# Optimization experiments

Measured on AMD Instinct MI355X. Metric: run time of the kernel, lower is better.

## Reference

```python
import jax, jax.numpy as jnp
import numpy as np

F = 64  # dim_features
DIM_TASK = 32


def setup_inputs() -> dict:
    key = jax.random.key(0)
    ks = jax.random.split(key, 16)
    n_state, n_task, n_actor = 65536, 32768, 32768
    E_st, E_ta = 2_000_000, 1_000_000
    inp = {
        'x_state': jax.random.normal(ks[0], (n_state, F), jnp.float32),
        'x_task': jax.random.normal(ks[1], (n_task, F), jnp.float32),
        'x_actor': jax.random.normal(ks[2], (n_actor, F), jnp.float32),
        'edge_attr': jax.random.normal(ks[3], (E_st, 2), jnp.float32),
        # GINEConv edge linear: Linear(2 -> F)
        'We': jax.random.normal(ks[4], (2, F), jnp.float32) * 0.5,
        'be': jnp.zeros((F,), jnp.float32),
        # GinStandardMLP: Linear(F,F) -> ReLU -> Linear(F,F)
        'W1a': jax.random.normal(ks[5], (F, F), jnp.float32) / np.sqrt(F),
        'b1a': jnp.zeros((F,), jnp.float32),
        'W1b': jax.random.normal(ks[6], (F, F), jnp.float32) / np.sqrt(F),
        'b1b': jnp.zeros((F,), jnp.float32),
        # UnactivatedMLP: Linear(F,F) -> ReLU -> Linear(F,1)
        'W2a': jax.random.normal(ks[7], (F, F), jnp.float32) / np.sqrt(F),
        'b2a': jnp.zeros((F,), jnp.float32),
        'W2b': jax.random.normal(ks[8], (F, 1), jnp.float32) / np.sqrt(F),
        'b2b': jnp.zeros((1,), jnp.float32),
        'src_st': jax.random.randint(ks[9], (E_st,), 0, n_state, jnp.int32),
        'dst_st': jax.random.randint(ks[10], (E_st,), 0, n_task, jnp.int32),
        'src_ta': jax.random.randint(ks[11], (E_ta,), 0, n_task, jnp.int32),
        'dst_ta': jax.random.randint(ks[12], (E_ta,), 0, n_actor, jnp.int32),
    }
    return inp


def reference(x_state, x_task, x_actor, edge_attr, We, be, W1a, b1a, W1b, b1b,
              W2a, b2a, W2b, b2b, src_st, dst_st, src_ta, dst_ta):
    n_task = x_task.shape[0]
    n_actor = x_actor.shape[0]
    # --- GINEConv (eps=0): agg_i = sum_e relu(x_src[e] + lin(edge_attr[e])) ---
    msg = jax.nn.relu(x_state[src_st] + edge_attr @ We + be)  # [E_st, F]
    agg = jax.ops.segment_sum(msg, dst_st, num_segments=n_task)  # [n_task, F]
    h = x_task + agg  # (1+eps)*x_r + agg, eps=0
    # GinStandardMLP: Linear-ReLU-Linear
    x1 = jax.nn.relu(h @ W1a + b1a) @ W1b + b1b  # [n_task, F]
    # --- GINConv (eps=0): agg2_i = sum_e x1[src[e]] ---
    agg2 = jax.ops.segment_sum(x1[src_ta], dst_ta, num_segments=n_actor)  # [n_actor, F]
    h2 = x_actor + agg2
    # UnactivatedMLP: Linear-ReLU-Linear -> 1
    logits = jax.nn.relu(h2 @ W2a + b2a) @ W2b + b2b  # [n_actor, 1]
    return logits.reshape(-1, DIM_TASK)
```

## Files before the change

### kernel.cpp

```cpp
#include <hip/hip_runtime.h>

#define F 64
#define TILE 8192
#define NB 1024
#define ROWSB 32
#define CAP1 2560
#define CAP2 1408
#define HS 68

#define WP1AH 0
#define WP1AL 4096
#define WP1BH 8192
#define WP1BL 12288
#define WP2AH 16384
#define WP2AL 20480

typedef __attribute__((ext_vector_type(8))) short bf8;
typedef __attribute__((ext_vector_type(4))) float f4;
typedef __attribute__((ext_vector_type(2))) float fl2;

__device__ __forceinline__ unsigned short f2bf(float f) {
    unsigned u = __float_as_uint(f);
    unsigned r = u + 0x7fffu + ((u >> 16) & 1u);
    return (unsigned short)(r >> 16);
}
__device__ __forceinline__ float bf2f(unsigned short h) {
    return __uint_as_float((unsigned)h << 16);
}
__device__ __forceinline__ fl2 unpack2(unsigned d) {
    fl2 r;
    r.x = __uint_as_float(d << 16);
    r.y = __uint_as_float(d & 0xffff0000u);
    return r;
}

__device__ __forceinline__ int block_scan_1024(int c, int tid, int* scratch) {
    int lane = tid & 63, wv = tid >> 6;
    int s = c;
    #pragma unroll
    for (int off = 1; off < 64; off <<= 1) {
        int u = __shfl_up(s, off);
        if (lane >= off) s += u;
    }
    if (lane == 63) scratch[wv] = s;
    __syncthreads();
    if (tid < 64) {
        int ws = (tid < 16) ? scratch[tid] : 0;
        int t = ws;
        #pragma unroll
        for (int off = 1; off < 16; off <<= 1) {
            int u = __shfl_up(t, off);
            if (tid >= off) t += u;
        }
        if (tid < 16) scratch[16 + tid] = t - ws;
    }
    __syncthreads();
    return s - c + scratch[16 + wv];
}

__global__ __launch_bounds__(1024) void prep_kernel(
    const float4* __restrict__ xs4, ushort4* __restrict__ xsb4, int n4,
    const int* __restrict__ src1, const int* __restrict__ dst1,
    const float* __restrict__ ea, int E1,
    int* __restrict__ cur1, uint2* __restrict__ keyA1,
    const int* __restrict__ src2, const int* __restrict__ dst2, int E2,
    int* __restrict__ cur2, unsigned* __restrict__ keyA2,
    const float* __restrict__ W1a, const float* __restrict__ W1b,
    const float* __restrict__ W2a, ushort* __restrict__ wp,
    int nBin1, int nBin2)
{
    __shared__ uint2 stage[TILE];
    __shared__ int hist[NB], lcur[NB], comb[NB];
    __shared__ int scratch[32];
    int bid = blockIdx.x;
    int tid = threadIdx.x;

    if (bid == 0) {
        int fid = tid & 511;
        int col = fid & 15, quad = (fid >> 4) & 3, c = (fid >> 6) & 3, kh = (fid >> 8) & 1;
        const float* Wsrc = (tid < 512) ? W1a : W1b;
        ushort* dh = wp + ((tid < 512) ? WP1AH : WP1BH);
        ushort* dl = wp + ((tid < 512) ? WP1AL : WP1BL);
        #pragma unroll
        for (int j = 0; j < 8; ++j) {
            int k = kh * 32 + quad * 8 + j;
            float w = Wsrc[k * F + c * 16 + col];
            unsigned short hi = f2bf(w);
            dh[fid * 8 + j] = hi;
            dl[fid * 8 + j] = f2bf(w - bf2f(hi));
        }
        if (tid < 512) {
            #pragma unroll
            for (int j = 0; j < 8; ++j) {
                int k = kh * 32 + quad * 8 + j;
                float w = W2a[k * F + c * 16 + col];
                unsigned short hi = f2bf(w);
                wp[WP2AH + fid * 8 + j] = hi;
                wp[WP2AL + fid * 8 + j] = f2bf(w - bf2f(hi));
            }
        }
        return;
    }

    if (bid <= nBin1) {
        int base = (bid - 1) * TILE;
        int cnt = min(TILE, E1 - base);
        hist[tid] = 0;
        __syncthreads();
        int myb[8]; unsigned msd[8], mpk[8];
        #pragma unroll
        for (int j = 0; j < 8; ++j) {
            int idx = tid + 1024 * j;
            if (idx < cnt) {
                int d = dst1[base + idx];
                int s = src1[base + idx];
                float2 e2 = ((const float2* __restrict__)ea)[base + idx];
                myb[j] = d >> 5;
                msd[j] = ((unsigned)s << 16) | (unsigned)d;
                mpk[j] = ((unsigned)f2bf(e2.y) << 16) | (unsigned)f2bf(e2.x);
                atomicAdd(&hist[myb[j]], 1);
            } else myb[j] = -1;
        }
        __syncthreads();
        int c = hist[tid];
        int gb = CAP1 * tid + atomicAdd(&cur1[tid], c);
        int excl = block_scan_1024(c, tid, scratch);
        comb[tid] = gb - excl;
        lcur[tid] = excl;
        __syncthreads();
        #pragma unroll
        for (int j = 0; j < 8; ++j) {
            if (myb[j] >= 0) {
                int p = atomicAdd(&lcur[myb[j]], 1);
                stage[p] = make_uint2(msd[j], mpk[j]);
            }
        }
        __syncthreads();
        #pragma unroll
        for (int j = 0; j < 8; ++j) {
            int p = tid + 1024 * j;
            if (p < cnt) {
                uint2 f = stage[p];
                int b = (int)(f.x & 0xffffu) >> 5;
                keyA1[comb[b] + p] = f;
            }
        }
        return;
    }

    if (bid <= nBin1 + nBin2) {
        unsigned* ustage = (unsigned*)stage;
        int base = (bid - 1 - nBin1) * TILE;
        int cnt = min(TILE, E2 - base);
        hist[tid] = 0;
        __syncthreads();
        int myb[8]; unsigned msd[8];
        #pragma unroll
        for (int j = 0; j < 8; ++j) {
            int idx = tid + 1024 * j;
            if (idx < cnt) {
                int d = dst2[base + idx];
                int s = src2[base + idx];
                myb[j] = d >> 5;
                msd[j] = ((unsigned)s << 16) | (unsigned)d;
                atomicAdd(&hist[myb[j]], 1);
            } else myb[j] = -1;
        }
        __syncthreads();
        int c = hist[tid];
        int gb = CAP2 * tid + atomicAdd(&cur2[tid], c);
        int excl = block_scan_1024(c, tid, scratch);
        comb[tid] = gb - excl;
        lcur[tid] = excl;
        __syncthreads();
        #pragma unroll
        for (int j = 0; j < 8; ++j) {
            if (myb[j] >= 0) {
                int p = atomicAdd(&lcur[myb[j]], 1);
                ustage[p] = msd[j];
            }
        }
        __syncthreads();
        #pragma unroll
        for (int j = 0; j < 8; ++j) {
            int p = tid + 1024 * j;
            if (p < cnt) {
                unsigned f = ustage[p];
                int b = (int)(f & 0xffffu) >> 5;
                keyA2[comb[b] + p] = f;
            }
        }
        return;
    }

    {
        int i = (bid - 1 - nBin1 - nBin2) * 1024 + tid;
        if (i < n4) {
            float4 v = xs4[i];
            ushort4 o;
            o.x = f2bf(v.x); o.y = f2bf(v.y); o.z = f2bf(v.z); o.w = f2bf(v.w);
            xsb4[i] = o;
        }
    }
}

__global__ __launch_bounds__(512) void sg1_kernel(
    const uint2* __restrict__ keyA,
    const ushort* __restrict__ xsb,
    const float* __restrict__ x_task,
    const float* __restrict__ We, const float* __restrict__ be,
    const int* __restrict__ gcursor,
    const ushort* __restrict__ wp,
    const float* __restrict__ b1a, const float* __restrict__ b1b,
    ushort* __restrict__ x1b, int n)
{
    __shared__ uint2 lpay[CAP1];
    __shared__ int hh[ROWSB], rst[ROWSB], cur[ROWSB];
    __shared__ float htile[ROWSB * HS];
    __shared__ float ltile[2 * 16 * HS];
    int tid = threadIdx.x;
    int b = blockIdx.x;
    int cnt = min(gcursor[b], CAP1);
    const uint2* ka = keyA + (size_t)b * CAP1;

    uint2 myk[5];
    #pragma unroll
    for (int j = 0; j < 5; ++j) {
        int idx = tid + 512 * j;
        if (idx < cnt) myk[j] = ka[idx];
    }
    if (tid < ROWSB) hh[tid] = 0;
    __syncthreads();
    #pragma unroll
    for (int j = 0; j < 5; ++j) {
        int idx = tid + 512 * j;
        if (idx < cnt) atomicAdd(&hh[myk[j].x & 31u], 1);
    }
    __syncthreads();
    if (tid < 64) {
        int cc = (tid < ROWSB) ? hh[tid] : 0;
        int s = cc;
        #pragma unroll
        for (int off = 1; off < ROWSB; off <<= 1) {
            int u = __shfl_up(s, off);
            if (tid >= off) s += u;
        }
        if (tid < ROWSB) { rst[tid] = s - cc; cur[tid] = s - cc; }
    }
    __syncthreads();
    #pragma unroll
    for (int j = 0; j < 5; ++j) {
        int idx = tid + 512 * j;
        if (idx < cnt) {
            int p = atomicAdd(&cur[myk[j].x & 31u], 1);
            lpay[p] = myk[j];
        }
    }
    __syncthreads();

    int wave = tid >> 6, lane = tid & 63;
    int q = lane & 7, g = lane >> 3;
    int gid = (wave << 3) | g;
    int r   = gid >> 1;
    int h   = gid & 1;
    int row = b * ROWSB + r;

    fl2 w0p[4], w1p[4], bbp[4];
    {
        float4 a0 = ((const float4* __restrict__)We)[q * 2];
        float4 a1 = ((const float4* __restrict__)We)[q * 2 + 1];
        float4 c0 = ((const float4* __restrict__)(We + F))[q * 2];
        float4 c1 = ((const float4* __restrict__)(We + F))[q * 2 + 1];
        float4 d0 = ((const float4* __restrict__)be)[q * 2];
        float4 d1 = ((const float4* __restrict__)be)[q * 2 + 1];
        w0p[0] = (fl2){a0.x, a0.y}; w0p[1] = (fl2){a0.z, a0.w};
        w0p[2] = (fl2){a1.x, a1.y}; w0p[3] = (fl2){a1.z, a1.w};
        w1p[0] = (fl2){c0.x, c0.y}; w1p[1] = (fl2){c0.z, c0.w};
        w1p[2] = (fl2){c1.x, c1.y}; w1p[3] = (fl2){c1.z, c1.w};
        bbp[0] = (fl2){d0.x, d0.y}; bbp[1] = (fl2){d0.z, d0.w};
        bbp[2] = (fl2){d1.x, d1.y}; bbp[3] = (fl2){d1.z, d1.w};
    }
    const fl2 zero2 = {0.f, 0.f};

    int c  = hh[r];
    int m0 = (c + 1) >> 1;
    int sh = rst[r] + (h ? m0 : 0);
    int m  = h ? (c - m0) : m0;

    fl2 acc2[4];
    #pragma unroll
    for (int p = 0; p < 4; ++p) acc2[p] = zero2;

    unsigned pk0 = 0, pk1 = 0, pk2 = 0, pk3 = 0;
    uint4 xw0 = {0,0,0,0}, xw1 = {0,0,0,0}, xw2 = {0,0,0,0}, xw3 = {0,0,0,0};

    #define SG1_LOAD(J, K)                                                          \
    if ((K) < m) {                                                                  \
        uint2 t = lpay[sh + (K)];                                                   \
        pk##J = t.y;                                                                \
        xw##J = ((const uint4* __restrict__)(xsb + ((size_t)(t.x >> 16) << 6)))[q]; \
    }

    #define SG1_COMP(PK, XW)                                                        \
    {                                                                               \
        fl2 ex = {__uint_as_float((PK) << 16), __uint_as_float((PK) << 16)};        \
        fl2 ey = {__uint_as_float((PK) & 0xffff0000u),                              \
                  __uint_as_float((PK) & 0xffff0000u)};                             \
        fl2 cc, t2;                                                                 \
        cc = __builtin_elementwise_fma(ey, w1p[0], bbp[0]);                         \
        cc = __builtin_elementwise_fma(ex, w0p[0], cc);                             \
        t2 = unpack2((XW).x) + cc;                                                  \
        acc2[0] += __builtin_elementwise_max(t2, zero2);                            \
        cc = __builtin_elementwise_fma(ey, w1p[1], bbp[1]);                         \
        cc = __builtin_elementwise_fma(ex, w0p[1], cc);                             \
        t2 = unpack2((XW).y) + cc;                                                  \
        acc2[1] += __builtin_elementwise_max(t2, zero2);                            \
        cc = __builtin_elementwise_fma(ey, w1p[2], bbp[2]);                         \
        cc = __builtin_elementwise_fma(ex, w0p[2], cc);                             \
        t2 = unpack2((XW).z) + cc;                                                  \
        acc2[2] += __builtin_elementwise_max(t2, zero2);                            \
        cc = __builtin_elementwise_fma(ey, w1p[3], bbp[3]);                         \
        cc = __builtin_elementwise_fma(ex, w0p[3], cc);                             \
        t2 = unpack2((XW).w) + cc;                                                  \
        acc2[3] += __builtin_elementwise_max(t2, zero2);                            \
    }

    SG1_LOAD(0, 0)
    SG1_LOAD(1, 1)
    SG1_LOAD(2, 2)
    SG1_LOAD(3, 3)
    int i = 0;
    for (; i + 4 <= m; i += 4) {
        SG1_COMP(pk0, xw0) SG1_LOAD(0, i + 4)
        SG1_COMP(pk1, xw1) SG1_LOAD(1, i + 5)
        SG1_COMP(pk2, xw2) SG1_LOAD(2, i + 6)
        SG1_COMP(pk3, xw3) SG1_LOAD(3, i + 7)
    }
    if (i < m)     SG1_COMP(pk0, xw0)
    if (i + 1 < m) SG1_COMP(pk1, xw1)
    if (i + 2 < m) SG1_COMP(pk2, xw2)
    #undef SG1_LOAD
    #undef SG1_COMP

    float acc[8];
    #pragma unroll
    for (int p = 0; p < 4; ++p) { acc[2 * p] = acc2[p].x; acc[2 * p + 1] = acc2[p].y; }
    #pragma unroll
    for (int j = 0; j < 8; ++j) acc[j] += __shfl_xor(acc[j], 8);

    if (h == 0 && row < n) {
        const float4* xt = (const float4* __restrict__)(x_task + (size_t)row * F + q * 8);
        float4 t0 = xt[0], t1 = xt[1];
        float4 o0, o1;
        o0.x = acc[0] + t0.x; o0.y = acc[1] + t0.y; o0.z = acc[2] + t0.z; o0.w = acc[3] + t0.w;
        o1.x = acc[4] + t1.x; o1.y = acc[5] + t1.y; o1.z = acc[6] + t1.z; o1.w = acc[7] + t1.w;
        float4* hp = (float4*)&htile[r * HS + q * 8];
        hp[0] = o0; hp[1] = o1;
    }
    __syncthreads();

    if (wave < 2) {
        int t = wave;
        int quad = lane >> 4, col = lane & 15;
        float* lt = ltile + t * 16 * HS;

        bf8 Ah[2], Al[2];
        #pragma unroll
        for (int kh = 0; kh < 2; ++kh) {
            const float4* hr4 = (const float4*)&htile[(t * 16 + col) * HS + kh * 32 + quad * 8];
            float4 v0 = hr4[0], v1 = hr4[1];
            float av[8] = {v0.x, v0.y, v0.z, v0.w, v1.x, v1.y, v1.z, v1.w};
            bf8 th, tl;
            #pragma unroll
            for (int j = 0; j < 8; ++j) {
                unsigned short h1 = f2bf(av[j]);
                th[j] = (short)h1; tl[j] = (short)f2bf(av[j] - bf2f(h1));
            }
            Ah[kh] = th; Al[kh] = tl;
        }
        #pragma unroll
        for (int c4i = 0; c4i < 4; ++c4i) {
            int f0 = ((0 * 4 + c4i) * 4 + quad) * 16 + col;
            int f1 = ((1 * 4 + c4i) * 4 + quad) * 16 + col;
            bf8 wh0 = *(const bf8*)(wp + WP1AH + f0 * 8);
            bf8 wl0 = *(const bf8*)(wp + WP1AL + f0 * 8);
            bf8 wh1 = *(const bf8*)(wp + WP1AH + f1 * 8);
            bf8 wl1 = *(const bf8*)(wp + WP1AL + f1 * 8);
            f4 accm = {0.f, 0.f, 0.f, 0.f};
            accm = __builtin_amdgcn_mfma_f32_16x16x32_bf16(Ah[0], wh0, accm, 0, 0, 0);
            accm = __builtin_amdgcn_mfma_f32_16x16x32_bf16(Ah[0], wl0, accm, 0, 0, 0);
            accm = __builtin_amdgcn_mfma_f32_16x16x32_bf16(Al[0], wh0, accm, 0, 0, 0);
            accm = __builtin_amdgcn_mfma_f32_16x16x32_bf16(Ah[1], wh1, accm, 0, 0, 0);
            accm = __builtin_amdgcn_mfma_f32_16x16x32_bf16(Ah[1], wl1, accm, 0, 0, 0);
            accm = __builtin_amdgcn_mfma_f32_16x16x32_bf16(Al[1], wh1, accm, 0, 0, 0);
            float ba = b1a[c4i * 16 + col];
            #pragma unroll
            for (int rr = 0; rr < 4; ++rr)
                lt[(quad * 4 + rr) * HS + c4i * 16 + col] = fmaxf(accm[rr] + ba, 0.f);
        }
        bf8 A2h[2], A2l[2];
        #pragma unroll
        for (int kh = 0; kh < 2; ++kh) {
            const float4* lr4 = (const float4*)&lt[col * HS + kh * 32 + quad * 8];
            float4 v0 = lr4[0], v1 = lr4[1];
            float av[8] = {v0.x, v0.y, v0.z, v0.w, v1.x, v1.y, v1.z, v1.w};
            bf8 th, tl;
            #pragma unroll
            for (int j = 0; j < 8; ++j) {
                unsigned short h1 = f2bf(av[j]);
                th[j] = (short)h1; tl[j] = (short)f2bf(av[j] - bf2f(h1));
            }
            A2h[kh] = th; A2l[kh] = tl;
        }
        #pragma unroll
        for (int c4i = 0; c4i < 4; ++c4i) {
            int f0 = ((0 * 4 + c4i) * 4 + quad) * 16 + col;
            int f1 = ((1 * 4 + c4i) * 4 + quad) * 16 + col;
            bf8 wh0 = *(const bf8*)(wp + WP1BH + f0 * 8);
            bf8 wl0 = *(const bf8*)(wp + WP1BL + f0 * 8);
            bf8 wh1 = *(const bf8*)(wp + WP1BH + f1 * 8);
            bf8 wl1 = *(const bf8*)(wp + WP1BL + f1 * 8);
            f4 accm = {0.f, 0.f, 0.f, 0.f};
            accm = __builtin_amdgcn_mfma_f32_16x16x32_bf16(A2h[0], wh0, accm, 0, 0, 0);
            accm = __builtin_amdgcn_mfma_f32_16x16x32_bf16(A2h[0], wl0, accm, 0, 0, 0);
            accm = __builtin_amdgcn_mfma_f32_16x16x32_bf16(A2l[0], wh0, accm, 0, 0, 0);
            accm = __builtin_amdgcn_mfma_f32_16x16x32_bf16(A2h[1], wh1, accm, 0, 0, 0);
            accm = __builtin_amdgcn_mfma_f32_16x16x32_bf16(A2h[1], wl1, accm, 0, 0, 0);
            accm = __builtin_amdgcn_mfma_f32_16x16x32_bf16(A2l[1], wh1, accm, 0, 0, 0);
            float bb = b1b[c4i * 16 + col];
            #pragma unroll
            for (int rr = 0; rr < 4; ++rr)
                lt[(quad * 4 + rr) * HS + c4i * 16 + col] = accm[rr] + bb;
        }
        int rr = lane >> 2, cc2 = (lane & 3) * 16;
        unsigned o[8];
        #pragma unroll
        for (int j = 0; j < 8; ++j) {
            unsigned lo = f2bf(lt[rr * HS + cc2 + 2 * j]);
            unsigned hi = f2bf(lt[rr * HS + cc2 + 2 * j + 1]);
            o[j] = lo | (hi << 16);
        }
        uint4* dst = (uint4*)(x1b + (size_t)(b * ROWSB + t * 16 + rr) * F + cc2);
        dst[0] = make_uint4(o[0], o[1], o[2], o[3]);
        dst[1] = make_uint4(o[4], o[5], o[6], o[7]);
    }
}

__global__ __launch_bounds__(512) void sg2_kernel(
    const unsigned* __restrict__ keyA,
    const ushort* __restrict__ x1b,
    const float* __restrict__ x_actor,
    const int* __restrict__ gcursor,
    const ushort* __restrict__ wp,
    const float* __restrict__ b2a, const float* __restrict__ W2b,
    const float* __restrict__ b2b,
    float* __restrict__ out, int n)
{
    __shared__ unsigned lpay[CAP2];
    __shared__ int hh[ROWSB], rst[ROWSB], cur[ROWSB];
    __shared__ float htile[ROWSB * HS];
    int tid = threadIdx.x;
    int b = blockIdx.x;
    int cnt = min(gcursor[b], CAP2);
    const unsigned* ka = keyA + (size_t)b * CAP2;

    unsigned myk[3];
    #pragma unroll
    for (int j = 0; j < 3; ++j) {
        int idx = tid + 512 * j;
        if (idx < cnt) myk[j] = ka[idx];
    }
    if (tid < ROWSB) hh[tid] = 0;
    __syncthreads();
    #pragma unroll
    for (int j = 0; j < 3; ++j) {
        int idx = tid + 512 * j;
        if (idx < cnt) atomicAdd(&hh[myk[j] & 31u], 1);
    }
    __syncthreads();
    if (tid < 64) {
        int cc = (tid < ROWSB) ? hh[tid] : 0;
        int s = cc;
        #pragma unroll
        for (int off = 1; off < ROWSB; off <<= 1) {
            int u = __shfl_up(s, off);
            if (tid >= off) s += u;
        }
        if (tid < ROWSB) { rst[tid] = s - cc; cur[tid] = s - cc; }
    }
    __syncthreads();
    #pragma unroll
    for (int j = 0; j < 3; ++j) {
        int idx = tid + 512 * j;
        if (idx < cnt) {
            int p = atomicAdd(&cur[myk[j] & 31u], 1);
            lpay[p] = myk[j];
        }
    }
    __syncthreads();

    int wave = tid >> 6, lane = tid & 63;
    int q = lane & 7, g = lane >> 3;
    int gid = (wave << 3) | g;
    int r   = gid >> 1;
    int h   = gid & 1;
    int row = b * ROWSB + r;
    const fl2 zero2 = {0.f, 0.f};

    int c  = hh[r];
    int m0 = (c + 1) >> 1;
    int sh = rst[r] + (h ? m0 : 0);
    int m  = h ? (c - m0) : m0;

    fl2 acc2[4];
    #pragma unroll
    for (int p = 0; p < 4; ++p) acc2[p] = zero2;

    uint4 xw0 = {0,0,0,0}, xw1 = {0,0,0,0}, xw2 = {0,0,0,0}, xw3 = {0,0,0,0};

    #define SG2_LOAD(J, K)                                                          \
    if ((K) < m) {                                                                  \
        unsigned t = lpay[sh + (K)];                                                \
        xw##J = ((const uint4* __restrict__)(x1b + ((size_t)(t >> 16) << 6)))[q];   \
    }

    #define SG2_COMP(XW)                                                            \
    {                                                                               \
        acc2[0] += unpack2((XW).x);                                                 \
        acc2[1] += unpack2((XW).y);                                                 \
        acc2[2] += unpack2((XW).z);                                                 \
        acc2[3] += unpack2((XW).w);                                                 \
    }

    SG2_LOAD(0, 0)
    SG2_LOAD(1, 1)
    SG2_LOAD(2, 2)
    SG2_LOAD(3, 3)
    int i = 0;
    for (; i + 4 <= m; i += 4) {
        SG2_COMP(xw0) SG2_LOAD(0, i + 4)
        SG2_COMP(xw1) SG2_LOAD(1, i + 5)
        SG2_COMP(xw2) SG2_LOAD(2, i + 6)
        SG2_COMP(xw3) SG2_LOAD(3, i + 7)
    }
    if (i < m)     SG2_COMP(xw0)
    if (i + 1 < m) SG2_COMP(xw1)
    if (i + 2 < m) SG2_COMP(xw2)
    #undef SG2_LOAD
    #undef SG2_COMP

    float acc[8];
    #pragma unroll
    for (int p = 0; p < 4; ++p) { acc[2 * p] = acc2[p].x; acc[2 * p + 1] = acc2[p].y; }
    #pragma unroll
    for (int j = 0; j < 8; ++j) acc[j] += __shfl_xor(acc[j], 8);

    if (h == 0 && row < n) {
        const float4* xt = (const float4* __restrict__)(x_actor + (size_t)row * F + q * 8);
        float4 t0 = xt[0], t1 = xt[1];
        float4 o0, o1;
        o0.x = acc[0] + t0.x; o0.y = acc[1] + t0.y; o0.z = acc[2] + t0.z; o0.w = acc[3] + t0.w;
        o1.x = acc[4] + t1.x; o1.y = acc[5] + t1.y; o1.z = acc[6] + t1.z; o1.w = acc[7] + t1.w;
        float4* hp = (float4*)&htile[r * HS + q * 8];
        hp[0] = o0; hp[1] = o1;
    }
    __syncthreads();

    if (wave < 2) {
        int t = wave;
        int quad = lane >> 4, col = lane & 15;

        bf8 Ah[2], Al[2];
        #pragma unroll
        for (int kh = 0; kh < 2; ++kh) {
            const float4* hr4 = (const float4*)&htile[(t * 16 + col) * HS + kh * 32 + quad * 8];
            float4 v0 = hr4[0], v1 = hr4[1];
            float av[8] = {v0.x, v0.y, v0.z, v0.w, v1.x, v1.y, v1.z, v1.w};
            bf8 th, tl;
            #pragma unroll
            for (int j = 0; j < 8; ++j) {
                unsigned short h1 = f2bf(av[j]);
                th[j] = (short)h1; tl[j] = (short)f2bf(av[j] - bf2f(h1));
            }
            Ah[kh] = th; Al[kh] = tl;
        }

        float partial[4] = {0.f, 0.f, 0.f, 0.f};
        #pragma unroll
        for (int c4i = 0; c4i < 4; ++c4i) {
            int f0 = ((0 * 4 + c4i) * 4 + quad) * 16 + col;
            int f1 = ((1 * 4 + c4i) * 4 + quad) * 16 + col;
            bf8 wh0 = *(const bf8*)(wp + WP2AH + f0 * 8);
            bf8 wl0 = *(const bf8*)(wp + WP2AL + f0 * 8);
            bf8 wh1 = *(const bf8*)(wp + WP2AH + f1 * 8);
            bf8 wl1 = *(const bf8*)(wp + WP2AL + f1 * 8);
            f4 accm = {0.f, 0.f, 0.f, 0.f};
            accm = __builtin_amdgcn_mfma_f32_16x16x32_bf16(Ah[0], wh0, accm, 0, 0, 0);
            accm = __builtin_amdgcn_mfma_f32_16x16x32_bf16(Ah[0], wl0, accm, 0, 0, 0);
            accm = __builtin_amdgcn_mfma_f32_16x16x32_bf16(Al[0], wh0, accm, 0, 0, 0);
            accm = __builtin_amdgcn_mfma_f32_16x16x32_bf16(Ah[1], wh1, accm, 0, 0, 0);
            accm = __builtin_amdgcn_mfma_f32_16x16x32_bf16(Ah[1], wl1, accm, 0, 0, 0);
            accm = __builtin_amdgcn_mfma_f32_16x16x32_bf16(Al[1], wh1, accm, 0, 0, 0);
            float ba = b2a[c4i * 16 + col];
            float w_o = W2b[c4i * 16 + col];
            #pragma unroll
            for (int rr = 0; rr < 4; ++rr)
                partial[rr] += fmaxf(accm[rr] + ba, 0.f) * w_o;
        }
        #pragma unroll
        for (int off = 1; off < 16; off <<= 1)
            #pragma unroll
            for (int rr = 0; rr < 4; ++rr)
                partial[rr] += __shfl_xor(partial[rr], off);
        if (col == 0) {
            float bias2 = b2b[0];
            #pragma unroll
            for (int rr = 0; rr < 4; ++rr)
                out[b * ROWSB + t * 16 + quad * 4 + rr] = partial[rr] + bias2;
        }
    }
}

extern "C" void kernel_launch(void* const* d_in, const int* in_sizes, int n_in,
                              void* d_out, int out_size, void* d_ws, size_t ws_size,
                              hipStream_t stream)
{
    const float* x_state   = (const float*)d_in[0];
    const float* x_task    = (const float*)d_in[1];
    const float* x_actor   = (const float*)d_in[2];
    const float* edge_attr = (const float*)d_in[3];
    const float* We        = (const float*)d_in[4];
    const float* be        = (const float*)d_in[5];
    const float* W1a       = (const float*)d_in[6];
    const float* b1a       = (const float*)d_in[7];
    const float* W1b       = (const float*)d_in[8];
    const float* b1b       = (const float*)d_in[9];
    const float* W2a       = (const float*)d_in[10];
    const float* b2a       = (const float*)d_in[11];
    const float* W2b       = (const float*)d_in[12];
    const float* b2b       = (const float*)d_in[13];
    const int*   src_st    = (const int*)d_in[14];
    const int*   dst_st    = (const int*)d_in[15];
    const int*   src_ta    = (const int*)d_in[16];
    const int*   dst_ta    = (const int*)d_in[17];

    int n_state = in_sizes[0] / F;
    int n_task  = in_sizes[1] / F;
    int n_actor = in_sizes[2] / F;
    int E_st    = in_sizes[14];
    int E_ta    = in_sizes[16];

    ushort*   x1b   = (ushort*)d_ws;
    float*    hbig  = (float*)(x1b + (size_t)n_task * F);
    ushort*   wp    = (ushort*)hbig;
    ushort*   xsb   = (ushort*)(hbig + (size_t)n_task * F);
    uint2*    keyA1 = (uint2*)(xsb + (size_t)n_state * F);
    unsigned* keyA2 = (unsigned*)(keyA1 + (size_t)NB * CAP1);
    int*      cur1  = (int*)(keyA2 + (size_t)NB * CAP2);
    int*      cur2  = cur1 + NB;

    int n4    = n_state * F / 4;
    int nCvt  = (n4 + 1023) / 1024;
    int nBin1 = (E_st + TILE - 1) / TILE;
    int nBin2 = (E_ta + TILE - 1) / TILE;

    hipMemsetAsync(cur1, 0, 2 * NB * sizeof(int), stream);
    prep_kernel<<<1 + nBin1 + nBin2 + nCvt, 1024, 0, stream>>>(
        (const float4*)x_state, (ushort4*)xsb, n4,
        src_st, dst_st, edge_attr, E_st, cur1, keyA1,
        src_ta, dst_ta, E_ta, cur2, keyA2,
        W1a, W1b, W2a, wp,
        nBin1, nBin2);
    sg1_kernel<<<NB, 512, 0, stream>>>(
        keyA1, xsb, x_task, We, be, cur1, wp, b1a, b1b, x1b, n_task);
    sg2_kernel<<<NB, 512, 0, stream>>>(
        keyA2, x1b, x_actor, cur2, wp, b2a, W2b, b2b, (float*)d_out, n_actor);
}
```

Baseline: 196.0 us.

## Move second-graph edge binning into sg1 kernel and split MLP across four waves

Edge binning for the task-to-actor graph moves out of the prep kernel and into extra leading blocks of the sg1 kernel, using a smaller 4096-edge tile and a 512-thread scan. The intent is to overlap that binning with the first graph's gather/MLP work and shorten the prep kernel. The per-block MLP now uses four waves, each computing half the output columns, with an added barrier between the two layers. Shared memory is manually carved from one buffer so both roles fit, which adds complexity and a risk of aliasing mistakes.

```diff
diff --git a/kernel.cpp b/kernel.cpp
--- a/kernel.cpp
+++ b/kernel.cpp
@@ -2,6 +2,7 @@
 
 #define F 64
 #define TILE 8192
+#define TILE2 4096
 #define NB 1024
 #define ROWSB 32
 #define CAP1 2560
@@ -58,16 +59,38 @@
     return s - c + scratch[16 + wv];
 }
 
+__device__ __forceinline__ int block_scan_512(int c, int tid, int* scratch) {
+    int lane = tid & 63, wv = tid >> 6;
+    int s = c;
+    #pragma unroll
+    for (int off = 1; off < 64; off <<= 1) {
+        int u = __shfl_up(s, off);
+        if (lane >= off) s += u;
+    }
+    if (lane == 63) scratch[wv] = s;
+    __syncthreads();
+    if (tid < 64) {
+        int ws = (tid < 8) ? scratch[tid] : 0;
+        int t = ws;
+        #pragma unroll
+        for (int off = 1; off < 8; off <<= 1) {
+            int u = __shfl_up(t, off);
+            if (tid >= off) t += u;
+        }
+        if (tid < 8) scratch[8 + tid] = t - ws;
+    }
+    __syncthreads();
+    return s - c + scratch[8 + wv];
+}
+
 __global__ __launch_bounds__(1024) void prep_kernel(
     const float4* __restrict__ xs4, ushort4* __restrict__ xsb4, int n4,
     const int* __restrict__ src1, const int* __restrict__ dst1,
     const float* __restrict__ ea, int E1,
     int* __restrict__ cur1, uint2* __restrict__ keyA1,
-    const int* __restrict__ src2, const int* __restrict__ dst2, int E2,
-    int* __restrict__ cur2, unsigned* __restrict__ keyA2,
     const float* __restrict__ W1a, const float* __restrict__ W1b,
     const float* __restrict__ W2a, ushort* __restrict__ wp,
-    int nBin1, int nBin2)
+    int nBin1)
 {
     __shared__ uint2 stage[TILE];
     __shared__ int hist[NB], lcur[NB], comb[NB];
@@ -148,53 +171,8 @@
         return;
     }
 
-    if (bid <= nBin1 + nBin2) {
-        unsigned* ustage = (unsigned*)stage;
-        int base = (bid - 1 - nBin1) * TILE;
-        int cnt = min(TILE, E2 - base);
-        hist[tid] = 0;
-        __syncthreads();
-        int myb[8]; unsigned msd[8];
-        #pragma unroll
-        for (int j = 0; j < 8; ++j) {
-            int idx = tid + 1024 * j;
-            if (idx < cnt) {
-                int d = dst2[base + idx];
-                int s = src2[base + idx];
-                myb[j] = d >> 5;
-                msd[j] = ((unsigned)s << 16) | (unsigned)d;
-                atomicAdd(&hist[myb[j]], 1);
-            } else myb[j] = -1;
-        }
-        __syncthreads();
-        int c = hist[tid];
-        int gb = CAP2 * tid + atomicAdd(&cur2[tid], c);
-        int excl = block_scan_1024(c, tid, scratch);
-        comb[tid] = gb - excl;
-        lcur[tid] = excl;
-        __syncthreads();
-        #pragma unroll
-        for (int j = 0; j < 8; ++j) {
-            if (myb[j] >= 0) {
-                int p = atomicAdd(&lcur[myb[j]], 1);
-                ustage[p] = msd[j];
-            }
-        }
-        __syncthreads();
-        #pragma unroll
-        for (int j = 0; j < 8; ++j) {
-            int p = tid + 1024 * j;
-            if (p < cnt) {
-                unsigned f = ustage[p];
-                int b = (int)(f & 0xffffu) >> 5;
-                keyA2[comb[b] + p] = f;
-            }
-        }
-        return;
-    }
-
     {
-        int i = (bid - 1 - nBin1 - nBin2) * 1024 + tid;
+        int i = (bid - 1 - nBin1) * 1024 + tid;
         if (i < n4) {
             float4 v = xs4[i];
             ushort4 o;
@@ -212,14 +190,73 @@
     const int* __restrict__ gcursor,
     const ushort* __restrict__ wp,
     const float* __restrict__ b1a, const float* __restrict__ b1b,
-    ushort* __restrict__ x1b, int n)
+    ushort* __restrict__ x1b, int n,
+    const int* __restrict__ src2, const int* __restrict__ dst2, int E2,
+    int* __restrict__ cur2, unsigned* __restrict__ keyA2, int nBin2b)
 {
-    __shared__ uint2 lpay[CAP1];
-    __shared__ int hh[ROWSB], rst[ROWSB], cur[ROWSB];
-    __shared__ float htile[ROWSB * HS];
-    __shared__ float ltile[2 * 16 * HS];
+    __shared__ __attribute__((aligned(16))) char smem[38272];
     int tid = threadIdx.x;
-    int b = blockIdx.x;
+    int bid = blockIdx.x;
+
+    if (bid < nBin2b) {
+        unsigned* ustage = (unsigned*)smem;
+        int* hist    = (int*)(smem + 16384);
+        int* lcur    = (int*)(smem + 20480);
+        int* comb    = (int*)(smem + 24576);
+        int* scratch = (int*)(smem + 28672);
+        int base = bid * TILE2;
+        int cnt2 = min(TILE2, E2 - base);
+        hist[tid] = 0; hist[tid + 512] = 0;
+        __syncthreads();
+        int myb[8]; unsigned msd[8];
+        #pragma unroll
+        for (int j = 0; j < 8; ++j) {
+            int idx = tid + 512 * j;
+            if (idx < cnt2) {
+                int d = dst2[base + idx];
+                int s = src2[base + idx];
+                myb[j] = d >> 5;
+                msd[j] = ((unsigned)s << 16) | (unsigned)d;
+                atomicAdd(&hist[myb[j]], 1);
+            } else myb[j] = -1;
+        }
+        __syncthreads();
+        int c0 = hist[2 * tid], c1 = hist[2 * tid + 1];
+        int excl = block_scan_512(c0 + c1, tid, scratch);
+        int gb0 = CAP2 * (2 * tid)     + atomicAdd(&cur2[2 * tid], c0);
+        int gb1 = CAP2 * (2 * tid + 1) + atomicAdd(&cur2[2 * tid + 1], c1);
+        comb[2 * tid]     = gb0 - excl;
+        comb[2 * tid + 1] = gb1 - (excl + c0);
+        lcur[2 * tid]     = excl;
+        lcur[2 * tid + 1] = excl + c0;
+        __syncthreads();
+        #pragma unroll
+        for (int j = 0; j < 8; ++j) {
+            if (myb[j] >= 0) {
+                int p = atomicAdd(&lcur[myb[j]], 1);
+                ustage[p] = msd[j];
+            }
+        }
+        __syncthreads();
+        #pragma unroll
+        for (int j = 0; j < 8; ++j) {
+            int p = tid + 512 * j;
+            if (p < cnt2) {
+                unsigned f = ustage[p];
+                int bkt = (int)(f & 0xffffu) >> 5;
+                keyA2[comb[bkt] + p] = f;
+            }
+        }
+        return;
+    }
+
+    int b = bid - nBin2b;
+    uint2* lpay  = (uint2*)smem;
+    int*   hh    = (int*)(smem + 20480);
+    int*   rst   = (int*)(smem + 20608);
+    int*   cur   = (int*)(smem + 20736);
+    float* htile = (float*)(smem + 20864);
+    float* ltile = (float*)(smem + 29568);
     int cnt = min(gcursor[b], CAP1);
     const uint2* ka = keyA + (size_t)b * CAP1;
 
@@ -359,12 +396,11 @@
     }
     __syncthreads();
 
-    if (wave < 2) {
-        int t = wave;
-        int quad = lane >> 4, col = lane & 15;
+    int quad = lane >> 4, col = lane & 15;
+    bf8 Ah[2], Al[2];
+    if (wave < 4) {
+        int t = wave >> 1, hc = wave & 1;
         float* lt = ltile + t * 16 * HS;
-
-        bf8 Ah[2], Al[2];
         #pragma unroll
         for (int kh = 0; kh < 2; ++kh) {
             const float4* hr4 = (const float4*)&htile[(t * 16 + col) * HS + kh * 32 + quad * 8];
@@ -379,9 +415,10 @@
             Ah[kh] = th; Al[kh] = tl;
         }
         #pragma unroll
-        for (int c4i = 0; c4i < 4; ++c4i) {
-            int f0 = ((0 * 4 + c4i) * 4 + quad) * 16 + col;
-            int f1 = ((1 * 4 + c4i) * 4 + quad) * 16 + col;
+        for (int cci = 0; cci < 2; ++cci) {
+            int c4i = 2 * hc + cci;
+            int f0 = (c4i * 4 + quad) * 16 + col;
+            int f1 = ((4 + c4i) * 4 + quad) * 16 + col;
             bf8 wh0 = *(const bf8*)(wp + WP1AH + f0 * 8);
             bf8 wl0 = *(const bf8*)(wp + WP1AL + f0 * 8);
             bf8 wh1 = *(const bf8*)(wp + WP1AH + f1 * 8);
@@ -398,6 +435,12 @@
             for (int rr = 0; rr < 4; ++rr)
                 lt[(quad * 4 + rr) * HS + c4i * 16 + col] = fmaxf(accm[rr] + ba, 0.f);
         }
+    }
+    __syncthreads();
+    if (wave < 4) {
+        int t = wave >> 1, hc = wave & 1;
+        float* lt = ltile + t * 16 * HS;
+        float* ot = htile + t * 16 * HS;
         bf8 A2h[2], A2l[2];
         #pragma unroll
         for (int kh = 0; kh < 2; ++kh) {
@@ -413,9 +456,10 @@
             A2h[kh] = th; A2l[kh] = tl;
         }
         #pragma unroll
-        for (int c4i = 0; c4i < 4; ++c4i) {
-            int f0 = ((0 * 4 + c4i) * 4 + quad) * 16 + col;
-            int f1 = ((1 * 4 + c4i) * 4 + quad) * 16 + col;
+        for (int cci = 0; cci < 2; ++cci) {
+            int c4i = 2 * hc + cci;
+            int f0 = (c4i * 4 + quad) * 16 + col;
+            int f1 = ((4 + c4i) * 4 + quad) * 16 + col;
             bf8 wh0 = *(const bf8*)(wp + WP1BH + f0 * 8);
             bf8 wl0 = *(const bf8*)(wp + WP1BL + f0 * 8);
             bf8 wh1 = *(const bf8*)(wp + WP1BH + f1 * 8);
@@ -430,19 +474,21 @@
             float bb = b1b[c4i * 16 + col];
             #pragma unroll
             for (int rr = 0; rr < 4; ++rr)
-                lt[(quad * 4 + rr) * HS + c4i * 16 + col] = accm[rr] + bb;
-        }
-        int rr = lane >> 2, cc2 = (lane & 3) * 16;
-        unsigned o[8];
-        #pragma unroll
-        for (int j = 0; j < 8; ++j) {
-            unsigned lo = f2bf(lt[rr * HS + cc2 + 2 * j]);
-            unsigned hi = f2bf(lt[rr * HS + cc2 + 2 * j + 1]);
-            o[j] = lo | (hi << 16);
-        }
-        uint4* dst = (uint4*)(x1b + (size_t)(b * ROWSB + t * 16 + rr) * F + cc2);
-        dst[0] = make_uint4(o[0], o[1], o[2], o[3]);
-        dst[1] = make_uint4(o[4], o[5], o[6], o[7]);
+                ot[(quad * 4 + rr) * HS + c4i * 16 + col] = accm[rr] + bb;
+        }
+        int rr2 = lane >> 2, gg = lane & 3;
+        if ((gg >> 1) == hc) {
+            unsigned o[8];
+            #pragma unroll
+            for (int j = 0; j < 8; ++j) {
+                unsigned lo = f2bf(ot[rr2 * HS + gg * 16 + 2 * j]);
+                unsigned hi = f2bf(ot[rr2 * HS + gg * 16 + 2 * j + 1]);
+                o[j] = lo | (hi << 16);
+            }
+            uint4* dst = (uint4*)(x1b + (size_t)(b * ROWSB + t * 16 + rr2) * F + gg * 16);
+            dst[0] = make_uint4(o[0], o[1], o[2], o[3]);
+            dst[1] = make_uint4(o[4], o[5], o[6], o[7]);
+        }
     }
 }
 
@@ -588,8 +634,8 @@
         float partial[4] = {0.f, 0.f, 0.f, 0.f};
         #pragma unroll
         for (int c4i = 0; c4i < 4; ++c4i) {
-            int f0 = ((0 * 4 + c4i) * 4 + quad) * 16 + col;
-            int f1 = ((1 * 4 + c4i) * 4 + quad) * 16 + col;
+            int f0 = (c4i * 4 + quad) * 16 + col;
+            int f1 = ((4 + c4i) * 4 + quad) * 16 + col;
             bf8 wh0 = *(const bf8*)(wp + WP2AH + f0 * 8);
             bf8 wl0 = *(const bf8*)(wp + WP2AL + f0 * 8);
             bf8 wh1 = *(const bf8*)(wp + WP2AH + f1 * 8);
@@ -659,20 +705,19 @@
     int*      cur1  = (int*)(keyA2 + (size_t)NB * CAP2);
     int*      cur2  = cur1 + NB;
 
-    int n4    = n_state * F / 4;
-    int nCvt  = (n4 + 1023) / 1024;
-    int nBin1 = (E_st + TILE - 1) / TILE;
-    int nBin2 = (E_ta + TILE - 1) / TILE;
+    int n4     = n_state * F / 4;
+    int nCvt   = (n4 + 1023) / 1024;
+    int nBin1  = (E_st + TILE - 1) / TILE;
+    int nBin2b = (E_ta + TILE2 - 1) / TILE2;
 
     hipMemsetAsync(cur1, 0, 2 * NB * sizeof(int), stream);
-    prep_kernel<<<1 + nBin1 + nBin2 + nCvt, 1024, 0, stream>>>(
+    prep_kernel<<<1 + nBin1 + nCvt, 1024, 0, stream>>>(
         (const float4*)x_state, (ushort4*)xsb, n4,
         src_st, dst_st, edge_attr, E_st, cur1, keyA1,
-        src_ta, dst_ta, E_ta, cur2, keyA2,
-        W1a, W1b, W2a, wp,
-        nBin1, nBin2);
-    sg1_kernel<<<NB, 512, 0, stream>>>(
-        keyA1, xsb, x_task, We, be, cur1, wp, b1a, b1b, x1b, n_task);
+        W1a, W1b, W2a, wp, nBin1);
+    sg1_kernel<<<nBin2b + NB, 512, 0, stream>>>(
+        keyA1, xsb, x_task, We, be, cur1, wp, b1a, b1b, x1b, n_task,
+        src_ta, dst_ta, E_ta, cur2, keyA2, nBin2b);
     sg2_kernel<<<NB, 512, 0, stream>>>(
         keyA2, x1b, x_actor, cur2, wp, b2a, W2b, b2b, (float*)d_out, n_actor);
 }
```

Measured after the change: 206.7 us. 1.05x slower.
